# Optimization experiments

Hardware: AMD Instinct MI355X
Metric: run time of the kernel (lower is better)

Reference implementation:

```python
import jax, jax.numpy as jnp
import numpy as np

N_NODES = 50000


def gcn_conv(x, edge_index, W, b, n):
    # PyG GCNConv: xW, add self-loops, symmetric degree normalization,
    # scatter-add messages from source (row) to target (col).
    xw = x @ W
    row, col = edge_index[0], edge_index[1]
    loops = jnp.arange(n, dtype=edge_index.dtype)
    row = jnp.concatenate([row, loops])
    col = jnp.concatenate([col, loops])
    deg = jax.ops.segment_sum(jnp.ones(row.shape[0], dtype=xw.dtype), col, num_segments=n)
    dinv = jnp.where(deg > 0, jax.lax.rsqrt(deg), 0.0)
    norm = dinv[row] * dinv[col]  # [E+N]
    out = jax.ops.segment_sum(xw[row] * norm[:, None], col, num_segments=n)
    return out + b


def setup_inputs() -> dict:
    key = jax.random.key(0)
    ks = jax.random.split(key, 5)
    n, d_in, d_h, d_out, n_edges = N_NODES, 128, 128, 4, 600000
    x = jax.random.normal(ks[0], (n, d_in), dtype=jnp.float32)
    edge_index = jax.random.randint(ks[1], (2, n_edges), 0, n, dtype=jnp.int64)
    W1 = jax.random.normal(ks[2], (d_in, d_h), dtype=jnp.float32) * (1.0 / np.sqrt(d_in))
    b1 = jnp.zeros((d_h,), dtype=jnp.float32)
    W2 = jax.random.normal(ks[3], (d_h, d_h), dtype=jnp.float32) * (1.0 / np.sqrt(d_h))
    b2 = jnp.zeros((d_h,), dtype=jnp.float32)
    Wfc = jax.random.normal(ks[4], (2 * d_h, d_out), dtype=jnp.float32) * (1.0 / np.sqrt(2 * d_h))
    bfc = jnp.zeros((d_out,), dtype=jnp.float32)
    return {"x": x, "edge_index": edge_index, "W1": W1, "b1": b1,
            "W2": W2, "b2": b2, "Wfc": Wfc, "bfc": bfc}


def reference(x, edge_index, W1, b1, W2, b2, Wfc, bfc):
    n = x.shape[0]
    # dropout is identity at inference (training=False)
    h = jax.nn.relu(gcn_conv(x, edge_index, W1, b1, n))
    h = jax.nn.relu(gcn_conv(h, edge_index, W2, b2, n))
    # edge-level gather + concat + linear classifier
    edge_x = jnp.concatenate([h[edge_index[0]], h[edge_index[1]]], axis=-1)  # [E, 2*d_h]
    edge_scores = edge_x @ Wfc + bfc  # [E, d_out]
    return jax.nn.log_softmax(edge_scores, axis=1)
```

## Files before the change

kernel.cpp:

```cpp
#include <hip/hip_runtime.h>
#include <math.h>
#include <stdint.h>

#define D 128
#define SCAN_CHUNK 2048
#define LDA 136

typedef __attribute__((ext_vector_type(8))) short v8s;
typedef __attribute__((ext_vector_type(4))) float v4f;

static __device__ __forceinline__ uint16_t f2bf(float f) {
    uint32_t u = __float_as_uint(f);
    u = (u + 0x7fff + ((u >> 16) & 1)) >> 16;
    return (uint16_t)u;
}
static __device__ __forceinline__ float bf2f(uint16_t h) { return __uint_as_float((uint32_t)h << 16); }
static __device__ __forceinline__ float bf_lo(uint32_t u) { return __uint_as_float(u << 16); }
static __device__ __forceinline__ float bf_hi(uint32_t u) { return __uint_as_float(u & 0xffff0000u); }


__global__ void countpack_kernel(const int* __restrict__ col, int* __restrict__ cnt,
                                 int* __restrict__ rnk, int E,
                                 const float* __restrict__ W1, const float* __restrict__ W2,
                                 uint16_t* __restrict__ Wh, uint16_t* __restrict__ Wl) {
    int tid = blockIdx.x * blockDim.x + threadIdx.x;
    if (tid < 2 * 16384) {
        int layer = tid >> 14;
        int li = tid & 16383;
        int j = li & 7, lane = (li >> 3) & 63, f = li >> 9;
        int kstep = f >> 3, tile = f & 7;
        int k = kstep * 32 + ((lane >> 4) * 8) + j;
        int nn = tile * 16 + (lane & 15);
        const float* W = layer ? W2 : W1;
        float v = W[k * 128 + nn];
        uint16_t h = f2bf(v);
        Wh[tid] = h;
        Wl[tid] = f2bf(v - bf2f(h));
    }
    if (tid < E) rnk[tid] = atomicAdd(&cnt[col[tid]], 1);
}


__global__ __launch_bounds__(256) void scanA_kernel(const int* __restrict__ cnt,
                                                    int* __restrict__ bsum,
                                                    float* __restrict__ dinv, int n) {
    __shared__ int wsum[4];
    int b = blockIdx.x, t = threadIdx.x;
    int base = b * SCAN_CHUNK;
    int s = 0;
#pragma unroll
    for (int k = 0; k < SCAN_CHUNK / 256; k++) {
        int i = base + k * 256 + t;
        if (i < n) {
            int c = cnt[i];
            s += c;
            dinv[i] = rsqrtf((float)c + 1.0f);
        }
    }
#pragma unroll
    for (int off = 32; off > 0; off >>= 1) s += __shfl_xor(s, off, 64);
    if ((t & 63) == 0) wsum[t >> 6] = s;
    __syncthreads();
    if (t == 0) bsum[b] = wsum[0] + wsum[1] + wsum[2] + wsum[3];
}


__global__ __launch_bounds__(256) void scanC_kernel(const int* __restrict__ cnt,
                                                    const int* __restrict__ bsum,
                                                    int* __restrict__ offs, int n, int nb) {
    __shared__ int stage[SCAN_CHUNK];
    __shared__ int res[SCAN_CHUNK];
    __shared__ int tsum[256];
    __shared__ int sb[64];
    int b = blockIdx.x, t = threadIdx.x;
    if (t < 64) {
        int v = (t < nb) ? bsum[t] : 0;
        int inc = v;
#pragma unroll
        for (int off = 1; off < 64; off <<= 1) {
            int u = __shfl_up(inc, off, 64);
            if (t >= off) inc += u;
        }
        sb[t] = inc;
    }
    int base = b * SCAN_CHUNK;
#pragma unroll
    for (int k = 0; k < SCAN_CHUNK / 256; k++) {
        int i = base + k * 256 + t;
        stage[k * 256 + t] = (i < n) ? cnt[i] : 0;
    }
    __syncthreads();
    int my = 0;
#pragma unroll
    for (int j = 0; j < 8; j++) my += stage[t * 8 + j];
    tsum[t] = my;
    __syncthreads();
    for (int off = 1; off < 256; off <<= 1) {
        int v = (t >= off) ? tsum[t - off] : 0;
        __syncthreads();
        tsum[t] += v;
        __syncthreads();
    }
    int bbase = (b == 0) ? 0 : sb[b - 1];
    int run = tsum[t] - my + bbase;
#pragma unroll
    for (int j = 0; j < 8; j++) {
        res[t * 8 + j] = run;
        run += stage[t * 8 + j];
    }
    __syncthreads();
#pragma unroll
    for (int k = 0; k < SCAN_CHUNK / 256; k++) {
        int i = base + k * 256 + t;
        if (i < n) offs[i] = res[k * 256 + t];
    }
    if (b == gridDim.x - 1 && t == 0) offs[n] = sb[nb - 1];
}


__global__ void fill_kernel(const int* __restrict__ row, const int* __restrict__ col,
                            const int* __restrict__ rnk, const int* __restrict__ offs,
                            int* __restrict__ adj, int E) {
    int e = blockIdx.x * blockDim.x + threadIdx.x;
    if (e < E) adj[offs[col[e]] + rnk[e]] = row[e];
}


__global__ __launch_bounds__(256) void gemm_mfma_kernel(const float* __restrict__ A,
                                                        const uint16_t* __restrict__ Wph,
                                                        const uint16_t* __restrict__ Wpl,
                                                        const float* __restrict__ dinv,
                                                        uint16_t* __restrict__ Cb, int M) {
    __shared__ uint16_t Ah[64][LDA];
    __shared__ uint16_t Al[64][LDA];
    int t = threadIdx.x;
    int base_row = blockIdx.x * 64;

#pragma unroll
    for (int kk = 0; kk < 8; kk++) {
        int idx = kk * 256 + t;
        int r = idx >> 5;
        int c4 = idx & 31;
        int gr = base_row + r;
        float4 f = (gr < M) ? *(const float4*)(A + (size_t)gr * D + c4 * 4)
                            : make_float4(0.f, 0.f, 0.f, 0.f);
        uint16_t h0 = f2bf(f.x), h1 = f2bf(f.y), h2 = f2bf(f.z), h3 = f2bf(f.w);
        uint16_t l0 = f2bf(f.x - bf2f(h0)), l1 = f2bf(f.y - bf2f(h1));
        uint16_t l2 = f2bf(f.z - bf2f(h2)), l3 = f2bf(f.w - bf2f(h3));
        *(ushort4*)&Ah[r][c4 * 4] = make_ushort4(h0, h1, h2, h3);
        *(ushort4*)&Al[r][c4 * 4] = make_ushort4(l0, l1, l2, l3);
    }
    __syncthreads();

    int lane = t & 63, w = t >> 6;
    int m_l = lane & 15, quad = lane >> 4;
    int arow = w * 16 + m_l;

    v4f acc[8];
#pragma unroll
    for (int i = 0; i < 8; i++) acc[i] = (v4f){0.f, 0.f, 0.f, 0.f};

#pragma unroll
    for (int ks = 0; ks < 4; ks++) {
        v8s ah = *(const v8s*)&Ah[arow][ks * 32 + quad * 8];
        v8s al = *(const v8s*)&Al[arow][ks * 32 + quad * 8];
#pragma unroll
        for (int ti = 0; ti < 8; ti++) {
            int f = ks * 8 + ti;
            v8s bh = *(const v8s*)(Wph + ((size_t)(f * 64 + lane)) * 8);
            v8s bl = *(const v8s*)(Wpl + ((size_t)(f * 64 + lane)) * 8);
            acc[ti] = __builtin_amdgcn_mfma_f32_16x16x32_bf16(al, bh, acc[ti], 0, 0, 0);
            acc[ti] = __builtin_amdgcn_mfma_f32_16x16x32_bf16(ah, bl, acc[ti], 0, 0, 0);
            acc[ti] = __builtin_amdgcn_mfma_f32_16x16x32_bf16(ah, bh, acc[ti], 0, 0, 0);
        }
    }

    int rbase = base_row + w * 16 + quad * 4;
#pragma unroll
    for (int reg = 0; reg < 4; reg++) {
        int gr = rbase + reg;
        if (gr < M) {
            float di = dinv[gr];
#pragma unroll
            for (int ti = 0; ti < 8; ti++) {
                Cb[(size_t)gr * D + ti * 16 + m_l] = f2bf(di * acc[ti][reg]);
            }
        }
    }
}


__global__ __launch_bounds__(256) void agg_kernel(const uint32_t* __restrict__ xwb,
                                                  const int* __restrict__ adj,
                                                  const int* __restrict__ offs,
                                                  const float* __restrict__ dinv,
                                                  const float* __restrict__ bias,
                                                  float* __restrict__ hout, int n) {
    int wave = (int)((blockIdx.x * (size_t)blockDim.x + threadIdx.x) >> 6);
    int lane = threadIdx.x & 63;
    if (wave >= n) return;
    int i = wave;
    uint32_t su = xwb[(size_t)i * (D / 2) + lane];
    float acc0 = bf_lo(su);
    float acc1 = bf_hi(su);
    int s = offs[i], e = offs[i + 1];
    int j = s;
    for (; j + 7 < e; j += 8) {
        int r0 = adj[j],     r1 = adj[j + 1], r2 = adj[j + 2], r3 = adj[j + 3];
        int r4 = adj[j + 4], r5 = adj[j + 5], r6 = adj[j + 6], r7 = adj[j + 7];
        uint32_t u0 = xwb[(size_t)r0 * (D / 2) + lane];
        uint32_t u1 = xwb[(size_t)r1 * (D / 2) + lane];
        uint32_t u2 = xwb[(size_t)r2 * (D / 2) + lane];
        uint32_t u3 = xwb[(size_t)r3 * (D / 2) + lane];
        uint32_t u4 = xwb[(size_t)r4 * (D / 2) + lane];
        uint32_t u5 = xwb[(size_t)r5 * (D / 2) + lane];
        uint32_t u6 = xwb[(size_t)r6 * (D / 2) + lane];
        uint32_t u7 = xwb[(size_t)r7 * (D / 2) + lane];
        acc0 += bf_lo(u0); acc1 += bf_hi(u0);
        acc0 += bf_lo(u1); acc1 += bf_hi(u1);
        acc0 += bf_lo(u2); acc1 += bf_hi(u2);
        acc0 += bf_lo(u3); acc1 += bf_hi(u3);
        acc0 += bf_lo(u4); acc1 += bf_hi(u4);
        acc0 += bf_lo(u5); acc1 += bf_hi(u5);
        acc0 += bf_lo(u6); acc1 += bf_hi(u6);
        acc0 += bf_lo(u7); acc1 += bf_hi(u7);
    }
    for (; j + 3 < e; j += 4) {
        int r0 = adj[j], r1 = adj[j + 1], r2 = adj[j + 2], r3 = adj[j + 3];
        uint32_t u0 = xwb[(size_t)r0 * (D / 2) + lane];
        uint32_t u1 = xwb[(size_t)r1 * (D / 2) + lane];
        uint32_t u2 = xwb[(size_t)r2 * (D / 2) + lane];
        uint32_t u3 = xwb[(size_t)r3 * (D / 2) + lane];
        acc0 += bf_lo(u0); acc1 += bf_hi(u0);
        acc0 += bf_lo(u1); acc1 += bf_hi(u1);
        acc0 += bf_lo(u2); acc1 += bf_hi(u2);
        acc0 += bf_lo(u3); acc1 += bf_hi(u3);
    }
    for (; j < e; j++) {
        int r = adj[j];
        uint32_t u = xwb[(size_t)r * (D / 2) + lane];
        acc0 += bf_lo(u); acc1 += bf_hi(u);
    }
    float di = dinv[i];
    float2 bv = ((const float2*)bias)[lane];
    float o0 = fmaxf(fmaf(di, acc0, bv.x), 0.f);
    float o1 = fmaxf(fmaf(di, acc1, bv.y), 0.f);
    ((float2*)(hout + (size_t)i * D))[lane] = make_float2(o0, o1);
}


__global__ __launch_bounds__(256) void agg2pq_kernel(const uint32_t* __restrict__ xwb,
                                                     const int* __restrict__ adj,
                                                     const int* __restrict__ offs,
                                                     const float* __restrict__ dinv,
                                                     const float* __restrict__ bias,
                                                     const float* __restrict__ Wfc,
                                                     const float* __restrict__ bfc,
                                                     float* __restrict__ P1,
                                                     float* __restrict__ P2, int n) {
    int wave = (int)((blockIdx.x * (size_t)blockDim.x + threadIdx.x) >> 6);
    int lane = threadIdx.x & 63;
    if (wave >= n) return;
    int i = wave;
    uint32_t su = xwb[(size_t)i * (D / 2) + lane];
    float acc0 = bf_lo(su);
    float acc1 = bf_hi(su);
    int s = offs[i], e = offs[i + 1];
    int j = s;
    for (; j + 7 < e; j += 8) {
        int r0 = adj[j],     r1 = adj[j + 1], r2 = adj[j + 2], r3 = adj[j + 3];
        int r4 = adj[j + 4], r5 = adj[j + 5], r6 = adj[j + 6], r7 = adj[j + 7];
        uint32_t u0 = xwb[(size_t)r0 * (D / 2) + lane];
        uint32_t u1 = xwb[(size_t)r1 * (D / 2) + lane];
        uint32_t u2 = xwb[(size_t)r2 * (D / 2) + lane];
        uint32_t u3 = xwb[(size_t)r3 * (D / 2) + lane];
        uint32_t u4 = xwb[(size_t)r4 * (D / 2) + lane];
        uint32_t u5 = xwb[(size_t)r5 * (D / 2) + lane];
        uint32_t u6 = xwb[(size_t)r6 * (D / 2) + lane];
        uint32_t u7 = xwb[(size_t)r7 * (D / 2) + lane];
        acc0 += bf_lo(u0); acc1 += bf_hi(u0);
        acc0 += bf_lo(u1); acc1 += bf_hi(u1);
        acc0 += bf_lo(u2); acc1 += bf_hi(u2);
        acc0 += bf_lo(u3); acc1 += bf_hi(u3);
        acc0 += bf_lo(u4); acc1 += bf_hi(u4);
        acc0 += bf_lo(u5); acc1 += bf_hi(u5);
        acc0 += bf_lo(u6); acc1 += bf_hi(u6);
        acc0 += bf_lo(u7); acc1 += bf_hi(u7);
    }
    for (; j + 3 < e; j += 4) {
        int r0 = adj[j], r1 = adj[j + 1], r2 = adj[j + 2], r3 = adj[j + 3];
        uint32_t u0 = xwb[(size_t)r0 * (D / 2) + lane];
        uint32_t u1 = xwb[(size_t)r1 * (D / 2) + lane];
        uint32_t u2 = xwb[(size_t)r2 * (D / 2) + lane];
        uint32_t u3 = xwb[(size_t)r3 * (D / 2) + lane];
        acc0 += bf_lo(u0); acc1 += bf_hi(u0);
        acc0 += bf_lo(u1); acc1 += bf_hi(u1);
        acc0 += bf_lo(u2); acc1 += bf_hi(u2);
        acc0 += bf_lo(u3); acc1 += bf_hi(u3);
    }
    for (; j < e; j++) {
        int r = adj[j];
        uint32_t u = xwb[(size_t)r * (D / 2) + lane];
        acc0 += bf_lo(u); acc1 += bf_hi(u);
    }
    float di = dinv[i];
    float2 bv = ((const float2*)bias)[lane];
    float o0 = fmaxf(fmaf(di, acc0, bv.x), 0.f);
    float o1 = fmaxf(fmaf(di, acc1, bv.y), 0.f);

    const float4* W4 = (const float4*)Wfc;
    float4 wa = W4[2 * lane];
    float4 wb = W4[2 * lane + 1];
    float4 wc = W4[128 + 2 * lane];
    float4 wd = W4[129 + 2 * lane];
    float p0 = fmaf(o0, wa.x, o1 * wb.x), p1 = fmaf(o0, wa.y, o1 * wb.y);
    float p2 = fmaf(o0, wa.z, o1 * wb.z), p3 = fmaf(o0, wa.w, o1 * wb.w);
    float q0 = fmaf(o0, wc.x, o1 * wd.x), q1 = fmaf(o0, wc.y, o1 * wd.y);
    float q2 = fmaf(o0, wc.z, o1 * wd.z), q3 = fmaf(o0, wc.w, o1 * wd.w);
#pragma unroll
    for (int off = 1; off < 64; off <<= 1) {
        p0 += __shfl_xor(p0, off, 64);
        p1 += __shfl_xor(p1, off, 64);
        p2 += __shfl_xor(p2, off, 64);
        p3 += __shfl_xor(p3, off, 64);
        q0 += __shfl_xor(q0, off, 64);
        q1 += __shfl_xor(q1, off, 64);
        q2 += __shfl_xor(q2, off, 64);
        q3 += __shfl_xor(q3, off, 64);
    }
    if (lane == 0) {
        float4 bb = *(const float4*)bfc;
        *(float4*)(P1 + (size_t)i * 4) = make_float4(p0 + bb.x, p1 + bb.y, p2 + bb.z, p3 + bb.w);
        *(float4*)(P2 + (size_t)i * 4) = make_float4(q0, q1, q2, q3);
    }
}


__global__ __launch_bounds__(256) void edge2_kernel(const int* __restrict__ row,
                                                    const int* __restrict__ col,
                                                    const float* __restrict__ P1,
                                                    const float* __restrict__ P2,
                                                    float* __restrict__ out, int E) {
    int e = blockIdx.x * blockDim.x + threadIdx.x;
    if (e >= E) return;
    int r = row[e], c = col[e];
    float4 a = ((const float4*)P1)[r];
    float4 b = ((const float4*)P2)[c];
    float sx = a.x + b.x, sy = a.y + b.y, sz = a.z + b.z, sw = a.w + b.w;
    float m = fmaxf(fmaxf(sx, sy), fmaxf(sz, sw));
    float e0 = expf(sx - m), e1 = expf(sy - m), e2 = expf(sz - m), e3 = expf(sw - m);
    float lse = m + logf(e0 + e1 + e2 + e3);
    *(float4*)(out + (size_t)e * 4) = make_float4(sx - lse, sy - lse, sz - lse, sw - lse);
}


extern "C" void kernel_launch(void* const* d_in, const int* in_sizes, int n_in,
                              void* d_out, int out_size, void* d_ws, size_t ws_size,
                              hipStream_t stream) {
    const float* x   = (const float*)d_in[0];
    const int*   ei  = (const int*)d_in[1];
    const float* W1  = (const float*)d_in[2];
    const float* b1  = (const float*)d_in[3];
    const float* W2  = (const float*)d_in[4];
    const float* b2  = (const float*)d_in[5];
    const float* Wfc = (const float*)d_in[6];
    const float* bfc = (const float*)d_in[7];
    float* out = (float*)d_out;

    int n = in_sizes[0] / D;
    int E = in_sizes[1] / 2;
    const int* row = ei;
    const int* col = ei + E;

    int nbScan = (n + SCAN_CHUNK - 1) / SCAN_CHUNK;

    uint16_t* xwb  = (uint16_t*)d_ws;
    float*    h    = (float*)(xwb + (size_t)n * D);
    int*      cnt  = (int*)(h + (size_t)n * D);
    int*      offs = cnt + n;
    int*      bsum = offs + (n + 4);
    int*      adj  = bsum + 64;
    int*      rnk  = adj + E;
    float*    dinv = (float*)(rnk + E);
    uint16_t* Wph  = (uint16_t*)(dinv + n);
    uint16_t* Wpl  = Wph + 2 * 16384;
    float*    P1   = (float*)(Wpl + 2 * 16384);
    float*    P2   = P1 + (size_t)n * 4;

    int nb_e = (E + 255) / 256;

    hipMemsetAsync(cnt, 0, (size_t)n * sizeof(int), stream);
    countpack_kernel<<<nb_e, 256, 0, stream>>>(col, cnt, rnk, E, W1, W2, Wph, Wpl);
    scanA_kernel<<<nbScan, 256, 0, stream>>>(cnt, bsum, dinv, n);
    scanC_kernel<<<nbScan, 256, 0, stream>>>(cnt, bsum, offs, n, nbScan);
    fill_kernel<<<nb_e, 256, 0, stream>>>(row, col, rnk, offs, adj, E);

    int nbG = (n + 63) / 64;

    gemm_mfma_kernel<<<nbG, 256, 0, stream>>>(x, Wph, Wpl, dinv, xwb, n);
    agg_kernel<<<(n + 3) / 4, 256, 0, stream>>>((const uint32_t*)xwb, adj, offs, dinv, b1, h, n);
    gemm_mfma_kernel<<<nbG, 256, 0, stream>>>(h, Wph + 16384, Wpl + 16384, dinv, xwb, n);
    agg2pq_kernel<<<(n + 3) / 4, 256, 0, stream>>>((const uint32_t*)xwb, adj, offs, dinv, b2,
                                                   Wfc, bfc, P1, P2, n);

    edge2_kernel<<<nb_e, 256, 0, stream>>>(row, col, P1, P2, out, E);
}
```

Baseline: 236.7 us.

## Fuse scan passes, fill with layer-1 GEMM, and layer-1 aggregation with layer-2 GEMM

Replaces the two-kernel block scan with a single 1024-thread block scan. CSR fill now shares a launch with the first GEMM as extra blocks, so the two run concurrently. Layer-1 aggregation writes its ReLU output as split bf16 straight into shared memory and feeds the layer-2 MFMA GEMM in the same block, which removes the fp32 h round trip and two launches. The risks are a serial single-block scan (about 49 elements per thread) and lower parallelism in the aggregation, since each wave now walks 16 rows one after another in 782 blocks.

```diff
diff --git a/kernel.cpp b/kernel.cpp
--- a/kernel.cpp
+++ b/kernel.cpp
@@ -3,7 +3,6 @@
 #include <stdint.h>
 
 #define D 128
-#define SCAN_CHUNK 2048
 #define LDA 136
 
 typedef __attribute__((ext_vector_type(8))) short v8s;
@@ -41,101 +40,104 @@
 }
 
 
-__global__ __launch_bounds__(256) void scanA_kernel(const int* __restrict__ cnt,
-                                                    int* __restrict__ bsum,
-                                                    float* __restrict__ dinv, int n) {
-    __shared__ int wsum[4];
-    int b = blockIdx.x, t = threadIdx.x;
-    int base = b * SCAN_CHUNK;
+__global__ __launch_bounds__(1024) void scan1_kernel(const int* __restrict__ cnt,
+                                                     int* __restrict__ offs,
+                                                     float* __restrict__ dinv, int n) {
+    __shared__ int tsum[1024];
+    int t = threadIdx.x;
+    int per = (n + 1023) / 1024;
+    int begin = t * per;
+    int end = begin + per; if (end > n) end = n;
     int s = 0;
-#pragma unroll
-    for (int k = 0; k < SCAN_CHUNK / 256; k++) {
-        int i = base + k * 256 + t;
-        if (i < n) {
-            int c = cnt[i];
-            s += c;
-            dinv[i] = rsqrtf((float)c + 1.0f);
-        }
-    }
-#pragma unroll
-    for (int off = 32; off > 0; off >>= 1) s += __shfl_xor(s, off, 64);
-    if ((t & 63) == 0) wsum[t >> 6] = s;
+    for (int i = begin; i < end; i++) {
+        int c = cnt[i];
+        s += c;
+        dinv[i] = rsqrtf((float)c + 1.0f);
+    }
+    tsum[t] = s;
     __syncthreads();
-    if (t == 0) bsum[b] = wsum[0] + wsum[1] + wsum[2] + wsum[3];
-}
-
-
-__global__ __launch_bounds__(256) void scanC_kernel(const int* __restrict__ cnt,
-                                                    const int* __restrict__ bsum,
-                                                    int* __restrict__ offs, int n, int nb) {
-    __shared__ int stage[SCAN_CHUNK];
-    __shared__ int res[SCAN_CHUNK];
-    __shared__ int tsum[256];
-    __shared__ int sb[64];
-    int b = blockIdx.x, t = threadIdx.x;
-    if (t < 64) {
-        int v = (t < nb) ? bsum[t] : 0;
-        int inc = v;
-#pragma unroll
-        for (int off = 1; off < 64; off <<= 1) {
-            int u = __shfl_up(inc, off, 64);
-            if (t >= off) inc += u;
-        }
-        sb[t] = inc;
-    }
-    int base = b * SCAN_CHUNK;
-#pragma unroll
-    for (int k = 0; k < SCAN_CHUNK / 256; k++) {
-        int i = base + k * 256 + t;
-        stage[k * 256 + t] = (i < n) ? cnt[i] : 0;
-    }
-    __syncthreads();
-    int my = 0;
-#pragma unroll
-    for (int j = 0; j < 8; j++) my += stage[t * 8 + j];
-    tsum[t] = my;
-    __syncthreads();
-    for (int off = 1; off < 256; off <<= 1) {
+    for (int off = 1; off < 1024; off <<= 1) {
         int v = (t >= off) ? tsum[t - off] : 0;
         __syncthreads();
         tsum[t] += v;
         __syncthreads();
     }
-    int bbase = (b == 0) ? 0 : sb[b - 1];
-    int run = tsum[t] - my + bbase;
-#pragma unroll
-    for (int j = 0; j < 8; j++) {
-        res[t * 8 + j] = run;
-        run += stage[t * 8 + j];
-    }
-    __syncthreads();
-#pragma unroll
-    for (int k = 0; k < SCAN_CHUNK / 256; k++) {
-        int i = base + k * 256 + t;
-        if (i < n) offs[i] = res[k * 256 + t];
-    }
-    if (b == gridDim.x - 1 && t == 0) offs[n] = sb[nb - 1];
-}
-
-
-__global__ void fill_kernel(const int* __restrict__ row, const int* __restrict__ col,
-                            const int* __restrict__ rnk, const int* __restrict__ offs,
-                            int* __restrict__ adj, int E) {
-    int e = blockIdx.x * blockDim.x + threadIdx.x;
-    if (e < E) adj[offs[col[e]] + rnk[e]] = row[e];
-}
-
-
-__global__ __launch_bounds__(256) void gemm_mfma_kernel(const float* __restrict__ A,
-                                                        const uint16_t* __restrict__ Wph,
-                                                        const uint16_t* __restrict__ Wpl,
-                                                        const float* __restrict__ dinv,
-                                                        uint16_t* __restrict__ Cb, int M) {
+    int run = tsum[t] - s;
+    for (int i = begin; i < end; i++) {
+        offs[i] = run;
+        run += cnt[i];
+    }
+    if (t == 1023) offs[n] = tsum[1023];
+}
+
+
+static __device__ __forceinline__ void gemm_body(const uint16_t Ah[][LDA],
+                                                 const uint16_t Al[][LDA],
+                                                 const uint16_t* __restrict__ Wph,
+                                                 const uint16_t* __restrict__ Wpl,
+                                                 const float* __restrict__ dinv,
+                                                 uint16_t* __restrict__ Cb,
+                                                 int base_row, int M, int t) {
+    int lane = t & 63, w = t >> 6;
+    int m_l = lane & 15, quad = lane >> 4;
+    int arow = w * 16 + m_l;
+
+    v4f acc[8];
+#pragma unroll
+    for (int i = 0; i < 8; i++) acc[i] = (v4f){0.f, 0.f, 0.f, 0.f};
+
+#pragma unroll
+    for (int ks = 0; ks < 4; ks++) {
+        v8s ah = *(const v8s*)&Ah[arow][ks * 32 + quad * 8];
+        v8s al = *(const v8s*)&Al[arow][ks * 32 + quad * 8];
+#pragma unroll
+        for (int ti = 0; ti < 8; ti++) {
+            int f = ks * 8 + ti;
+            v8s bh = *(const v8s*)(Wph + ((size_t)(f * 64 + lane)) * 8);
+            v8s bl = *(const v8s*)(Wpl + ((size_t)(f * 64 + lane)) * 8);
+            acc[ti] = __builtin_amdgcn_mfma_f32_16x16x32_bf16(al, bh, acc[ti], 0, 0, 0);
+            acc[ti] = __builtin_amdgcn_mfma_f32_16x16x32_bf16(ah, bl, acc[ti], 0, 0, 0);
+            acc[ti] = __builtin_amdgcn_mfma_f32_16x16x32_bf16(ah, bh, acc[ti], 0, 0, 0);
+        }
+    }
+
+    int rbase = base_row + w * 16 + quad * 4;
+#pragma unroll
+    for (int reg = 0; reg < 4; reg++) {
+        int gr = rbase + reg;
+        if (gr < M) {
+            float di = dinv[gr];
+#pragma unroll
+            for (int ti = 0; ti < 8; ti++) {
+                Cb[(size_t)gr * D + ti * 16 + m_l] = f2bf(di * acc[ti][reg]);
+            }
+        }
+    }
+}
+
+
+__global__ __launch_bounds__(256) void fillgemm_kernel(const int* __restrict__ row,
+                                                       const int* __restrict__ col,
+                                                       const int* __restrict__ rnk,
+                                                       const int* __restrict__ offs,
+                                                       int* __restrict__ adj, int E,
+                                                       const float* __restrict__ A,
+                                                       const uint16_t* __restrict__ Wph,
+                                                       const uint16_t* __restrict__ Wpl,
+                                                       const float* __restrict__ dinv,
+                                                       uint16_t* __restrict__ Cb, int M,
+                                                       int nbG) {
     __shared__ uint16_t Ah[64][LDA];
     __shared__ uint16_t Al[64][LDA];
     int t = threadIdx.x;
+
+    if (blockIdx.x >= nbG) {
+        int e = (blockIdx.x - nbG) * 256 + t;
+        if (e < E) adj[offs[col[e]] + rnk[e]] = row[e];
+        return;
+    }
+
     int base_row = blockIdx.x * 64;
-
 #pragma unroll
     for (int kk = 0; kk < 8; kk++) {
         int idx = kk * 256 + t;
@@ -151,101 +153,81 @@
         *(ushort4*)&Al[r][c4 * 4] = make_ushort4(l0, l1, l2, l3);
     }
     __syncthreads();
-
-    int lane = t & 63, w = t >> 6;
-    int m_l = lane & 15, quad = lane >> 4;
-    int arow = w * 16 + m_l;
-
-    v4f acc[8];
-#pragma unroll
-    for (int i = 0; i < 8; i++) acc[i] = (v4f){0.f, 0.f, 0.f, 0.f};
-
-#pragma unroll
-    for (int ks = 0; ks < 4; ks++) {
-        v8s ah = *(const v8s*)&Ah[arow][ks * 32 + quad * 8];
-        v8s al = *(const v8s*)&Al[arow][ks * 32 + quad * 8];
-#pragma unroll
-        for (int ti = 0; ti < 8; ti++) {
-            int f = ks * 8 + ti;
-            v8s bh = *(const v8s*)(Wph + ((size_t)(f * 64 + lane)) * 8);
-            v8s bl = *(const v8s*)(Wpl + ((size_t)(f * 64 + lane)) * 8);
-            acc[ti] = __builtin_amdgcn_mfma_f32_16x16x32_bf16(al, bh, acc[ti], 0, 0, 0);
-            acc[ti] = __builtin_amdgcn_mfma_f32_16x16x32_bf16(ah, bl, acc[ti], 0, 0, 0);
-            acc[ti] = __builtin_amdgcn_mfma_f32_16x16x32_bf16(ah, bh, acc[ti], 0, 0, 0);
+    gemm_body(Ah, Al, Wph, Wpl, dinv, Cb, base_row, M, t);
+}
+
+
+__global__ __launch_bounds__(256) void agggemm_kernel(const uint32_t* __restrict__ xwb,
+                                                      const int* __restrict__ adj,
+                                                      const int* __restrict__ offs,
+                                                      const float* __restrict__ dinv,
+                                                      const float* __restrict__ bias,
+                                                      const uint16_t* __restrict__ Wph,
+                                                      const uint16_t* __restrict__ Wpl,
+                                                      uint16_t* __restrict__ Cb, int M) {
+    __shared__ uint16_t Ah[64][LDA];
+    __shared__ uint16_t Al[64][LDA];
+    int t = threadIdx.x, lane = t & 63, w = t >> 6;
+    int base_row = blockIdx.x * 64;
+    float2 bv = ((const float2*)bias)[lane];
+
+    for (int rr = 0; rr < 16; rr++) {
+        int r = w * 16 + rr;
+        int i = base_row + r;
+        float o0 = 0.f, o1 = 0.f;
+        if (i < M) {
+            uint32_t su = xwb[(size_t)i * (D / 2) + lane];
+            float acc0 = bf_lo(su);
+            float acc1 = bf_hi(su);
+            int s = offs[i], e = offs[i + 1];
+            int j = s;
+            for (; j + 7 < e; j += 8) {
+                int r0 = adj[j],     r1 = adj[j + 1], r2 = adj[j + 2], r3 = adj[j + 3];
+                int r4 = adj[j + 4], r5 = adj[j + 5], r6 = adj[j + 6], r7 = adj[j + 7];
+                uint32_t u0 = xwb[(size_t)r0 * (D / 2) + lane];
+                uint32_t u1 = xwb[(size_t)r1 * (D / 2) + lane];
+                uint32_t u2 = xwb[(size_t)r2 * (D / 2) + lane];
+                uint32_t u3 = xwb[(size_t)r3 * (D / 2) + lane];
+                uint32_t u4 = xwb[(size_t)r4 * (D / 2) + lane];
+                uint32_t u5 = xwb[(size_t)r5 * (D / 2) + lane];
+                uint32_t u6 = xwb[(size_t)r6 * (D / 2) + lane];
+                uint32_t u7 = xwb[(size_t)r7 * (D / 2) + lane];
+                acc0 += bf_lo(u0); acc1 += bf_hi(u0);
+                acc0 += bf_lo(u1); acc1 += bf_hi(u1);
+                acc0 += bf_lo(u2); acc1 += bf_hi(u2);
+                acc0 += bf_lo(u3); acc1 += bf_hi(u3);
+                acc0 += bf_lo(u4); acc1 += bf_hi(u4);
+                acc0 += bf_lo(u5); acc1 += bf_hi(u5);
+                acc0 += bf_lo(u6); acc1 += bf_hi(u6);
+                acc0 += bf_lo(u7); acc1 += bf_hi(u7);
+            }
+            for (; j + 3 < e; j += 4) {
+                int r0 = adj[j], r1 = adj[j + 1], r2 = adj[j + 2], r3 = adj[j + 3];
+                uint32_t u0 = xwb[(size_t)r0 * (D / 2) + lane];
+                uint32_t u1 = xwb[(size_t)r1 * (D / 2) + lane];
+                uint32_t u2 = xwb[(size_t)r2 * (D / 2) + lane];
+                uint32_t u3 = xwb[(size_t)r3 * (D / 2) + lane];
+                acc0 += bf_lo(u0); acc1 += bf_hi(u0);
+                acc0 += bf_lo(u1); acc1 += bf_hi(u1);
+                acc0 += bf_lo(u2); acc1 += bf_hi(u2);
+                acc0 += bf_lo(u3); acc1 += bf_hi(u3);
+            }
+            for (; j < e; j++) {
+                int rx = adj[j];
+                uint32_t u = xwb[(size_t)rx * (D / 2) + lane];
+                acc0 += bf_lo(u); acc1 += bf_hi(u);
+            }
+            float di = dinv[i];
+            o0 = fmaxf(fmaf(di, acc0, bv.x), 0.f);
+            o1 = fmaxf(fmaf(di, acc1, bv.y), 0.f);
         }
-    }
-
-    int rbase = base_row + w * 16 + quad * 4;
-#pragma unroll
-    for (int reg = 0; reg < 4; reg++) {
-        int gr = rbase + reg;
-        if (gr < M) {
-            float di = dinv[gr];
-#pragma unroll
-            for (int ti = 0; ti < 8; ti++) {
-                Cb[(size_t)gr * D + ti * 16 + m_l] = f2bf(di * acc[ti][reg]);
-            }
-        }
-    }
-}
-
-
-__global__ __launch_bounds__(256) void agg_kernel(const uint32_t* __restrict__ xwb,
-                                                  const int* __restrict__ adj,
-                                                  const int* __restrict__ offs,
-                                                  const float* __restrict__ dinv,
-                                                  const float* __restrict__ bias,
-                                                  float* __restrict__ hout, int n) {
-    int wave = (int)((blockIdx.x * (size_t)blockDim.x + threadIdx.x) >> 6);
-    int lane = threadIdx.x & 63;
-    if (wave >= n) return;
-    int i = wave;
-    uint32_t su = xwb[(size_t)i * (D / 2) + lane];
-    float acc0 = bf_lo(su);
-    float acc1 = bf_hi(su);
-    int s = offs[i], e = offs[i + 1];
-    int j = s;
-    for (; j + 7 < e; j += 8) {
-        int r0 = adj[j],     r1 = adj[j + 1], r2 = adj[j + 2], r3 = adj[j + 3];
-        int r4 = adj[j + 4], r5 = adj[j + 5], r6 = adj[j + 6], r7 = adj[j + 7];
-        uint32_t u0 = xwb[(size_t)r0 * (D / 2) + lane];
-        uint32_t u1 = xwb[(size_t)r1 * (D / 2) + lane];
-        uint32_t u2 = xwb[(size_t)r2 * (D / 2) + lane];
-        uint32_t u3 = xwb[(size_t)r3 * (D / 2) + lane];
-        uint32_t u4 = xwb[(size_t)r4 * (D / 2) + lane];
-        uint32_t u5 = xwb[(size_t)r5 * (D / 2) + lane];
-        uint32_t u6 = xwb[(size_t)r6 * (D / 2) + lane];
-        uint32_t u7 = xwb[(size_t)r7 * (D / 2) + lane];
-        acc0 += bf_lo(u0); acc1 += bf_hi(u0);
-        acc0 += bf_lo(u1); acc1 += bf_hi(u1);
-        acc0 += bf_lo(u2); acc1 += bf_hi(u2);
-        acc0 += bf_lo(u3); acc1 += bf_hi(u3);
-        acc0 += bf_lo(u4); acc1 += bf_hi(u4);
-        acc0 += bf_lo(u5); acc1 += bf_hi(u5);
-        acc0 += bf_lo(u6); acc1 += bf_hi(u6);
-        acc0 += bf_lo(u7); acc1 += bf_hi(u7);
-    }
-    for (; j + 3 < e; j += 4) {
-        int r0 = adj[j], r1 = adj[j + 1], r2 = adj[j + 2], r3 = adj[j + 3];
-        uint32_t u0 = xwb[(size_t)r0 * (D / 2) + lane];
-        uint32_t u1 = xwb[(size_t)r1 * (D / 2) + lane];
-        uint32_t u2 = xwb[(size_t)r2 * (D / 2) + lane];
-        uint32_t u3 = xwb[(size_t)r3 * (D / 2) + lane];
-        acc0 += bf_lo(u0); acc1 += bf_hi(u0);
-        acc0 += bf_lo(u1); acc1 += bf_hi(u1);
-        acc0 += bf_lo(u2); acc1 += bf_hi(u2);
-        acc0 += bf_lo(u3); acc1 += bf_hi(u3);
-    }
-    for (; j < e; j++) {
-        int r = adj[j];
-        uint32_t u = xwb[(size_t)r * (D / 2) + lane];
-        acc0 += bf_lo(u); acc1 += bf_hi(u);
-    }
-    float di = dinv[i];
-    float2 bv = ((const float2*)bias)[lane];
-    float o0 = fmaxf(fmaf(di, acc0, bv.x), 0.f);
-    float o1 = fmaxf(fmaf(di, acc1, bv.y), 0.f);
-    ((float2*)(hout + (size_t)i * D))[lane] = make_float2(o0, o1);
+        uint16_t h0 = f2bf(o0), h1 = f2bf(o1);
+        uint16_t l0 = f2bf(o0 - bf2f(h0)), l1 = f2bf(o1 - bf2f(h1));
+        *(ushort2*)&Ah[r][2 * lane] = make_ushort2(h0, h1);
+        *(ushort2*)&Al[r][2 * lane] = make_ushort2(l0, l1);
+    }
+    __syncthreads();
+    gemm_body(Ah, Al, Wph, Wpl, dinv, Cb, base_row, M, t);
 }
 
 
@@ -372,14 +354,11 @@
     const int* row = ei;
     const int* col = ei + E;
 
-    int nbScan = (n + SCAN_CHUNK - 1) / SCAN_CHUNK;
-
     uint16_t* xwb  = (uint16_t*)d_ws;
-    float*    h    = (float*)(xwb + (size_t)n * D);
-    int*      cnt  = (int*)(h + (size_t)n * D);
+    uint16_t* xwb2 = xwb + (size_t)n * D;
+    int*      cnt  = (int*)(xwb2 + (size_t)n * D);
     int*      offs = cnt + n;
-    int*      bsum = offs + (n + 4);
-    int*      adj  = bsum + 64;
+    int*      adj  = offs + (n + 4);
     int*      rnk  = adj + E;
     float*    dinv = (float*)(rnk + E);
     uint16_t* Wph  = (uint16_t*)(dinv + n);
@@ -388,19 +367,19 @@
     float*    P2   = P1 + (size_t)n * 4;
 
     int nb_e = (E + 255) / 256;
+    int nbG  = (n + 63) / 64;
 
     hipMemsetAsync(cnt, 0, (size_t)n * sizeof(int), stream);
     countpack_kernel<<<nb_e, 256, 0, stream>>>(col, cnt, rnk, E, W1, W2, Wph, Wpl);
-    scanA_kernel<<<nbScan, 256, 0, stream>>>(cnt, bsum, dinv, n);
-    scanC_kernel<<<nbScan, 256, 0, stream>>>(cnt, bsum, offs, n, nbScan);
-    fill_kernel<<<nb_e, 256, 0, stream>>>(row, col, rnk, offs, adj, E);
-
-    int nbG = (n + 63) / 64;
-
-    gemm_mfma_kernel<<<nbG, 256, 0, stream>>>(x, Wph, Wpl, dinv, xwb, n);
-    agg_kernel<<<(n + 3) / 4, 256, 0, stream>>>((const uint32_t*)xwb, adj, offs, dinv, b1, h, n);
-    gemm_mfma_kernel<<<nbG, 256, 0, stream>>>(h, Wph + 16384, Wpl + 16384, dinv, xwb, n);
-    agg2pq_kernel<<<(n + 3) / 4, 256, 0, stream>>>((const uint32_t*)xwb, adj, offs, dinv, b2,
+    scan1_kernel<<<1, 1024, 0, stream>>>(cnt, offs, dinv, n);
+
+    fillgemm_kernel<<<nbG + nb_e, 256, 0, stream>>>(row, col, rnk, offs, adj, E,
+                                                    x, Wph, Wpl, dinv, xwb, n, nbG);
+
+    agggemm_kernel<<<nbG, 256, 0, stream>>>((const uint32_t*)xwb, adj, offs, dinv, b1,
+                                            Wph + 16384, Wpl + 16384, xwb2, n);
+
+    agg2pq_kernel<<<(n + 3) / 4, 256, 0, stream>>>((const uint32_t*)xwb2, adj, offs, dinv, b2,
                                                    Wfc, bfc, P1, P2, n);
 
     edge2_kernel<<<nb_e, 256, 0, stream>>>(row, col, P1, P2, out, E);
```

New measurement: 363.1 us. 1.53x slower.

## Fuse CSR fill with first GEMM and layer-1 aggregation with second GEMM

Applied to the files above, without the earlier changes.

Merges the adjacency fill into the first GEMM launch by adding extra blocks that do the scatter, and fuses the layer-1 aggregation, bias and ReLU directly into the second GEMM. The aggregated rows are written to LDS as bf16 hi/lo splits instead of a float h buffer in global memory. This removes two kernel launches and the global round trip of the intermediate hidden features. In exchange, the fused aggregation runs only 4 waves per 64 rows, each handling 16 rows two at a time, which lowers parallelism for the latency-bound gather.

```diff
diff --git a/kernel.cpp b/kernel.cpp
--- a/kernel.cpp
+++ b/kernel.cpp
@@ -118,24 +118,73 @@
 }
 
 
-__global__ void fill_kernel(const int* __restrict__ row, const int* __restrict__ col,
-                            const int* __restrict__ rnk, const int* __restrict__ offs,
-                            int* __restrict__ adj, int E) {
-    int e = blockIdx.x * blockDim.x + threadIdx.x;
-    if (e < E) adj[offs[col[e]] + rnk[e]] = row[e];
-}
-
-
-__global__ __launch_bounds__(256) void gemm_mfma_kernel(const float* __restrict__ A,
-                                                        const uint16_t* __restrict__ Wph,
-                                                        const uint16_t* __restrict__ Wpl,
-                                                        const float* __restrict__ dinv,
-                                                        uint16_t* __restrict__ Cb, int M) {
+static __device__ __forceinline__ void gemm_body(const uint16_t Ah[][LDA],
+                                                 const uint16_t Al[][LDA],
+                                                 const uint16_t* __restrict__ Wph,
+                                                 const uint16_t* __restrict__ Wpl,
+                                                 const float* __restrict__ dinv,
+                                                 uint16_t* __restrict__ Cb,
+                                                 int base_row, int M, int t) {
+    int lane = t & 63, w = t >> 6;
+    int m_l = lane & 15, quad = lane >> 4;
+    int arow = w * 16 + m_l;
+
+    v4f acc[8];
+#pragma unroll
+    for (int i = 0; i < 8; i++) acc[i] = (v4f){0.f, 0.f, 0.f, 0.f};
+
+#pragma unroll
+    for (int ks = 0; ks < 4; ks++) {
+        v8s ah = *(const v8s*)&Ah[arow][ks * 32 + quad * 8];
+        v8s al = *(const v8s*)&Al[arow][ks * 32 + quad * 8];
+#pragma unroll
+        for (int ti = 0; ti < 8; ti++) {
+            int f = ks * 8 + ti;
+            v8s bh = *(const v8s*)(Wph + ((size_t)(f * 64 + lane)) * 8);
+            v8s bl = *(const v8s*)(Wpl + ((size_t)(f * 64 + lane)) * 8);
+            acc[ti] = __builtin_amdgcn_mfma_f32_16x16x32_bf16(al, bh, acc[ti], 0, 0, 0);
+            acc[ti] = __builtin_amdgcn_mfma_f32_16x16x32_bf16(ah, bl, acc[ti], 0, 0, 0);
+            acc[ti] = __builtin_amdgcn_mfma_f32_16x16x32_bf16(ah, bh, acc[ti], 0, 0, 0);
+        }
+    }
+
+    int rbase = base_row + w * 16 + quad * 4;
+#pragma unroll
+    for (int reg = 0; reg < 4; reg++) {
+        int gr = rbase + reg;
+        if (gr < M) {
+            float di = dinv[gr];
+#pragma unroll
+            for (int ti = 0; ti < 8; ti++) {
+                Cb[(size_t)gr * D + ti * 16 + m_l] = f2bf(di * acc[ti][reg]);
+            }
+        }
+    }
+}
+
+
+__global__ __launch_bounds__(256) void fillgemm_kernel(const int* __restrict__ row,
+                                                       const int* __restrict__ col,
+                                                       const int* __restrict__ rnk,
+                                                       const int* __restrict__ offs,
+                                                       int* __restrict__ adj, int E,
+                                                       const float* __restrict__ A,
+                                                       const uint16_t* __restrict__ Wph,
+                                                       const uint16_t* __restrict__ Wpl,
+                                                       const float* __restrict__ dinv,
+                                                       uint16_t* __restrict__ Cb, int M,
+                                                       int nbG) {
     __shared__ uint16_t Ah[64][LDA];
     __shared__ uint16_t Al[64][LDA];
     int t = threadIdx.x;
+
+    if (blockIdx.x >= nbG) {
+        int e = (blockIdx.x - nbG) * 256 + t;
+        if (e < E) adj[offs[col[e]] + rnk[e]] = row[e];
+        return;
+    }
+
     int base_row = blockIdx.x * 64;
-
 #pragma unroll
     for (int kk = 0; kk < 8; kk++) {
         int idx = kk * 256 + t;
@@ -151,101 +200,123 @@
         *(ushort4*)&Al[r][c4 * 4] = make_ushort4(l0, l1, l2, l3);
     }
     __syncthreads();
-
-    int lane = t & 63, w = t >> 6;
-    int m_l = lane & 15, quad = lane >> 4;
-    int arow = w * 16 + m_l;
-
-    v4f acc[8];
-#pragma unroll
-    for (int i = 0; i < 8; i++) acc[i] = (v4f){0.f, 0.f, 0.f, 0.f};
-
-#pragma unroll
-    for (int ks = 0; ks < 4; ks++) {
-        v8s ah = *(const v8s*)&Ah[arow][ks * 32 + quad * 8];
-        v8s al = *(const v8s*)&Al[arow][ks * 32 + quad * 8];
-#pragma unroll
-        for (int ti = 0; ti < 8; ti++) {
-            int f = ks * 8 + ti;
-            v8s bh = *(const v8s*)(Wph + ((size_t)(f * 64 + lane)) * 8);
-            v8s bl = *(const v8s*)(Wpl + ((size_t)(f * 64 + lane)) * 8);
-            acc[ti] = __builtin_amdgcn_mfma_f32_16x16x32_bf16(al, bh, acc[ti], 0, 0, 0);
-            acc[ti] = __builtin_amdgcn_mfma_f32_16x16x32_bf16(ah, bl, acc[ti], 0, 0, 0);
-            acc[ti] = __builtin_amdgcn_mfma_f32_16x16x32_bf16(ah, bh, acc[ti], 0, 0, 0);
-        }
-    }
-
-    int rbase = base_row + w * 16 + quad * 4;
-#pragma unroll
-    for (int reg = 0; reg < 4; reg++) {
-        int gr = rbase + reg;
-        if (gr < M) {
-            float di = dinv[gr];
-#pragma unroll
-            for (int ti = 0; ti < 8; ti++) {
-                Cb[(size_t)gr * D + ti * 16 + m_l] = f2bf(di * acc[ti][reg]);
+    gemm_body(Ah, Al, Wph, Wpl, dinv, Cb, base_row, M, t);
+}
+
+
+__global__ __launch_bounds__(256) void agggemm_kernel(const uint32_t* __restrict__ xwb,
+                                                      const int* __restrict__ adj,
+                                                      const int* __restrict__ offs,
+                                                      const float* __restrict__ dinv,
+                                                      const float* __restrict__ bias,
+                                                      const uint16_t* __restrict__ Wph,
+                                                      const uint16_t* __restrict__ Wpl,
+                                                      uint16_t* __restrict__ Cb, int M) {
+    __shared__ uint16_t Ah[64][LDA];
+    __shared__ uint16_t Al[64][LDA];
+    int t = threadIdx.x, lane = t & 63, w = t >> 6;
+    int base_row = blockIdx.x * 64;
+    float2 bv = ((const float2*)bias)[lane];
+
+    for (int rr = 0; rr < 8; rr++) {
+        int rA = w * 16 + rr, rB = rA + 8;
+        int iA = base_row + rA, iB = base_row + rB;
+        float a0 = 0.f, a1 = 0.f, c0 = 0.f, c1 = 0.f;
+        int jA = 0, eA = 0, jB = 0, eB = 0;
+        if (iA < M) {
+            uint32_t su = xwb[(size_t)iA * (D / 2) + lane];
+            a0 = bf_lo(su); a1 = bf_hi(su);
+            jA = offs[iA]; eA = offs[iA + 1];
+        }
+        if (iB < M) {
+            uint32_t su = xwb[(size_t)iB * (D / 2) + lane];
+            c0 = bf_lo(su); c1 = bf_hi(su);
+            jB = offs[iB]; eB = offs[iB + 1];
+        }
+        while (jA + 7 < eA && jB + 7 < eB) {
+            int xx[8], yy[8];
+#pragma unroll
+            for (int q = 0; q < 8; q++) { xx[q] = adj[jA + q]; yy[q] = adj[jB + q]; }
+            uint32_t uA[8], uB[8];
+#pragma unroll
+            for (int q = 0; q < 8; q++) {
+                uA[q] = xwb[(size_t)xx[q] * (D / 2) + lane];
+                uB[q] = xwb[(size_t)yy[q] * (D / 2) + lane];
             }
-        }
-    }
-}
-
-
-__global__ __launch_bounds__(256) void agg_kernel(const uint32_t* __restrict__ xwb,
-                                                  const int* __restrict__ adj,
-                                                  const int* __restrict__ offs,
-                                                  const float* __restrict__ dinv,
-                                                  const float* __restrict__ bias,
-                                                  float* __restrict__ hout, int n) {
-    int wave = (int)((blockIdx.x * (size_t)blockDim.x + threadIdx.x) >> 6);
-    int lane = threadIdx.x & 63;
-    if (wave >= n) return;
-    int i = wave;
-    uint32_t su = xwb[(size_t)i * (D / 2) + lane];
-    float acc0 = bf_lo(su);
-    float acc1 = bf_hi(su);
-    int s = offs[i], e = offs[i + 1];
-    int j = s;
-    for (; j + 7 < e; j += 8) {
-        int r0 = adj[j],     r1 = adj[j + 1], r2 = adj[j + 2], r3 = adj[j + 3];
-        int r4 = adj[j + 4], r5 = adj[j + 5], r6 = adj[j + 6], r7 = adj[j + 7];
-        uint32_t u0 = xwb[(size_t)r0 * (D / 2) + lane];
-        uint32_t u1 = xwb[(size_t)r1 * (D / 2) + lane];
-        uint32_t u2 = xwb[(size_t)r2 * (D / 2) + lane];
-        uint32_t u3 = xwb[(size_t)r3 * (D / 2) + lane];
-        uint32_t u4 = xwb[(size_t)r4 * (D / 2) + lane];
-        uint32_t u5 = xwb[(size_t)r5 * (D / 2) + lane];
-        uint32_t u6 = xwb[(size_t)r6 * (D / 2) + lane];
-        uint32_t u7 = xwb[(size_t)r7 * (D / 2) + lane];
-        acc0 += bf_lo(u0); acc1 += bf_hi(u0);
-        acc0 += bf_lo(u1); acc1 += bf_hi(u1);
-        acc0 += bf_lo(u2); acc1 += bf_hi(u2);
-        acc0 += bf_lo(u3); acc1 += bf_hi(u3);
-        acc0 += bf_lo(u4); acc1 += bf_hi(u4);
-        acc0 += bf_lo(u5); acc1 += bf_hi(u5);
-        acc0 += bf_lo(u6); acc1 += bf_hi(u6);
-        acc0 += bf_lo(u7); acc1 += bf_hi(u7);
-    }
-    for (; j + 3 < e; j += 4) {
-        int r0 = adj[j], r1 = adj[j + 1], r2 = adj[j + 2], r3 = adj[j + 3];
-        uint32_t u0 = xwb[(size_t)r0 * (D / 2) + lane];
-        uint32_t u1 = xwb[(size_t)r1 * (D / 2) + lane];
-        uint32_t u2 = xwb[(size_t)r2 * (D / 2) + lane];
-        uint32_t u3 = xwb[(size_t)r3 * (D / 2) + lane];
-        acc0 += bf_lo(u0); acc1 += bf_hi(u0);
-        acc0 += bf_lo(u1); acc1 += bf_hi(u1);
-        acc0 += bf_lo(u2); acc1 += bf_hi(u2);
-        acc0 += bf_lo(u3); acc1 += bf_hi(u3);
-    }
-    for (; j < e; j++) {
-        int r = adj[j];
-        uint32_t u = xwb[(size_t)r * (D / 2) + lane];
-        acc0 += bf_lo(u); acc1 += bf_hi(u);
-    }
-    float di = dinv[i];
-    float2 bv = ((const float2*)bias)[lane];
-    float o0 = fmaxf(fmaf(di, acc0, bv.x), 0.f);
-    float o1 = fmaxf(fmaf(di, acc1, bv.y), 0.f);
-    ((float2*)(hout + (size_t)i * D))[lane] = make_float2(o0, o1);
+#pragma unroll
+            for (int q = 0; q < 8; q++) {
+                a0 += bf_lo(uA[q]); a1 += bf_hi(uA[q]);
+                c0 += bf_lo(uB[q]); c1 += bf_hi(uB[q]);
+            }
+            jA += 8; jB += 8;
+        }
+        for (; jA + 7 < eA; jA += 8) {
+            int xx[8]; uint32_t uA[8];
+#pragma unroll
+            for (int q = 0; q < 8; q++) xx[q] = adj[jA + q];
+#pragma unroll
+            for (int q = 0; q < 8; q++) uA[q] = xwb[(size_t)xx[q] * (D / 2) + lane];
+#pragma unroll
+            for (int q = 0; q < 8; q++) { a0 += bf_lo(uA[q]); a1 += bf_hi(uA[q]); }
+        }
+        for (; jA + 3 < eA; jA += 4) {
+            int x0 = adj[jA], x1 = adj[jA + 1], x2 = adj[jA + 2], x3 = adj[jA + 3];
+            uint32_t u0 = xwb[(size_t)x0 * (D / 2) + lane];
+            uint32_t u1 = xwb[(size_t)x1 * (D / 2) + lane];
+            uint32_t u2 = xwb[(size_t)x2 * (D / 2) + lane];
+            uint32_t u3 = xwb[(size_t)x3 * (D / 2) + lane];
+            a0 += bf_lo(u0); a1 += bf_hi(u0);
+            a0 += bf_lo(u1); a1 += bf_hi(u1);
+            a0 += bf_lo(u2); a1 += bf_hi(u2);
+            a0 += bf_lo(u3); a1 += bf_hi(u3);
+        }
+        for (; jA < eA; jA++) {
+            uint32_t u = xwb[(size_t)adj[jA] * (D / 2) + lane];
+            a0 += bf_lo(u); a1 += bf_hi(u);
+        }
+        for (; jB + 7 < eB; jB += 8) {
+            int yy[8]; uint32_t uB[8];
+#pragma unroll
+            for (int q = 0; q < 8; q++) yy[q] = adj[jB + q];
+#pragma unroll
+            for (int q = 0; q < 8; q++) uB[q] = xwb[(size_t)yy[q] * (D / 2) + lane];
+#pragma unroll
+            for (int q = 0; q < 8; q++) { c0 += bf_lo(uB[q]); c1 += bf_hi(uB[q]); }
+        }
+        for (; jB + 3 < eB; jB += 4) {
+            int y0 = adj[jB], y1 = adj[jB + 1], y2 = adj[jB + 2], y3 = adj[jB + 3];
+            uint32_t u0 = xwb[(size_t)y0 * (D / 2) + lane];
+            uint32_t u1 = xwb[(size_t)y1 * (D / 2) + lane];
+            uint32_t u2 = xwb[(size_t)y2 * (D / 2) + lane];
+            uint32_t u3 = xwb[(size_t)y3 * (D / 2) + lane];
+            c0 += bf_lo(u0); c1 += bf_hi(u0);
+            c0 += bf_lo(u1); c1 += bf_hi(u1);
+            c0 += bf_lo(u2); c1 += bf_hi(u2);
+            c0 += bf_lo(u3); c1 += bf_hi(u3);
+        }
+        for (; jB < eB; jB++) {
+            uint32_t u = xwb[(size_t)adj[jB] * (D / 2) + lane];
+            c0 += bf_lo(u); c1 += bf_hi(u);
+        }
+        float diA = (iA < M) ? dinv[iA] : 0.f;
+        float diB = (iB < M) ? dinv[iB] : 0.f;
+        float oA0 = fmaxf(fmaf(diA, a0, bv.x), 0.f);
+        float oA1 = fmaxf(fmaf(diA, a1, bv.y), 0.f);
+        float oB0 = fmaxf(fmaf(diB, c0, bv.x), 0.f);
+        float oB1 = fmaxf(fmaf(diB, c1, bv.y), 0.f);
+        if (iA >= M) { oA0 = 0.f; oA1 = 0.f; }
+        if (iB >= M) { oB0 = 0.f; oB1 = 0.f; }
+        uint16_t hA0 = f2bf(oA0), hA1 = f2bf(oA1);
+        uint16_t lA0 = f2bf(oA0 - bf2f(hA0)), lA1 = f2bf(oA1 - bf2f(hA1));
+        uint16_t hB0 = f2bf(oB0), hB1 = f2bf(oB1);
+        uint16_t lB0 = f2bf(oB0 - bf2f(hB0)), lB1 = f2bf(oB1 - bf2f(hB1));
+        *(ushort2*)&Ah[rA][2 * lane] = make_ushort2(hA0, hA1);
+        *(ushort2*)&Al[rA][2 * lane] = make_ushort2(lA0, lA1);
+        *(ushort2*)&Ah[rB][2 * lane] = make_ushort2(hB0, hB1);
+        *(ushort2*)&Al[rB][2 * lane] = make_ushort2(lB0, lB1);
+    }
+    __syncthreads();
+    gemm_body(Ah, Al, Wph, Wpl, dinv, Cb, base_row, M, t);
 }
 
 
@@ -375,8 +446,8 @@
     int nbScan = (n + SCAN_CHUNK - 1) / SCAN_CHUNK;
 
     uint16_t* xwb  = (uint16_t*)d_ws;
-    float*    h    = (float*)(xwb + (size_t)n * D);
-    int*      cnt  = (int*)(h + (size_t)n * D);
+    uint16_t* xwb2 = xwb + (size_t)n * D;
+    int*      cnt  = (int*)(xwb2 + (size_t)n * D);
     int*      offs = cnt + n;
     int*      bsum = offs + (n + 4);
     int*      adj  = bsum + 64;
@@ -388,19 +459,20 @@
     float*    P2   = P1 + (size_t)n * 4;
 
     int nb_e = (E + 255) / 256;
+    int nbG  = (n + 63) / 64;
 
     hipMemsetAsync(cnt, 0, (size_t)n * sizeof(int), stream);
     countpack_kernel<<<nb_e, 256, 0, stream>>>(col, cnt, rnk, E, W1, W2, Wph, Wpl);
     scanA_kernel<<<nbScan, 256, 0, stream>>>(cnt, bsum, dinv, n);
     scanC_kernel<<<nbScan, 256, 0, stream>>>(cnt, bsum, offs, n, nbScan);
-    fill_kernel<<<nb_e, 256, 0, stream>>>(row, col, rnk, offs, adj, E);
-
-    int nbG = (n + 63) / 64;
-
-    gemm_mfma_kernel<<<nbG, 256, 0, stream>>>(x, Wph, Wpl, dinv, xwb, n);
-    agg_kernel<<<(n + 3) / 4, 256, 0, stream>>>((const uint32_t*)xwb, adj, offs, dinv, b1, h, n);
-    gemm_mfma_kernel<<<nbG, 256, 0, stream>>>(h, Wph + 16384, Wpl + 16384, dinv, xwb, n);
-    agg2pq_kernel<<<(n + 3) / 4, 256, 0, stream>>>((const uint32_t*)xwb, adj, offs, dinv, b2,
+
+    fillgemm_kernel<<<nbG + nb_e, 256, 0, stream>>>(row, col, rnk, offs, adj, E,
+                                                    x, Wph, Wpl, dinv, xwb, n, nbG);
+
+    agggemm_kernel<<<nbG, 256, 0, stream>>>((const uint32_t*)xwb, adj, offs, dinv, b1,
+                                            Wph + 16384, Wpl + 16384, xwb2, n);
+
+    agg2pq_kernel<<<(n + 3) / 4, 256, 0, stream>>>((const uint32_t*)xwb2, adj, offs, dinv, b2,
                                                    Wfc, bfc, P1, P2, n);
 
     edge2_kernel<<<nb_e, 256, 0, stream>>>(row, col, P1, P2, out, E);
```

Measured after the change: 235.7 us. About the same (-0.4%).
